# Optimization experiments

Hardware: AMD Instinct MI355X
Metric: run time of the kernel (lower is better)

Reference implementation:

```python
import jax, jax.numpy as jnp
import numpy as np

N, E, H, HEADS, L, B = 16000, 256000, 192, 4, 4, 8
C = H // HEADS
VN, VE, T = 32, 8, 1000


def _sin_emb(t, dim):
    half = dim // 2
    freqs = jnp.exp(-np.log(10000.0) * jnp.arange(half, dtype=jnp.float32) / half)
    ang = t.astype(jnp.float32)[:, None] * freqs[None, :]
    return jnp.concatenate([jnp.sin(ang), jnp.cos(ang)], axis=-1)


def _ln(x, g, b, eps=1e-5):
    mu = jnp.mean(x, -1, keepdims=True)
    var = jnp.mean(jnp.square(x - mu), -1, keepdims=True)
    return (x - mu) * jax.lax.rsqrt(var + eps) * g + b


def setup_inputs():
    key = jax.random.key(0)
    ks = iter(jax.random.split(key, 64))
    p = lambda shape, s=0.02: jax.random.normal(next(ks), shape, jnp.float32) * s
    inp = {}
    inp['node_emb'] = p((VN, H))
    inp['edge_emb'] = p((VE, H))
    inp['time_w1'] = p((H, H)); inp['time_b1'] = jnp.zeros((H,), jnp.float32)
    inp['time_w2'] = p((H, H)); inp['time_b2'] = jnp.zeros((H,), jnp.float32)
    inp['mask_emb'] = p((2, H))
    inp['wq'] = p((L, H, H)); inp['bq'] = jnp.zeros((L, H), jnp.float32)
    inp['wk'] = p((L, H, H)); inp['bk'] = jnp.zeros((L, H), jnp.float32)
    inp['wv'] = p((L, H, H)); inp['bv'] = jnp.zeros((L, H), jnp.float32)
    inp['we'] = p((L, H, H))
    inp['wskip'] = p((L, H, H)); inp['bskip'] = jnp.zeros((L, H), jnp.float32)
    inp['wbeta'] = p((L, 3 * H))
    inp['ln_g'] = jnp.ones((L, H), jnp.float32); inp['ln_b'] = jnp.zeros((L, H), jnp.float32)
    inp['node_out_w'] = p((H, VN)); inp['node_out_b'] = jnp.zeros((VN,), jnp.float32)
    inp['edge_w1'] = p((4 * H, H)); inp['edge_b1'] = jnp.zeros((H,), jnp.float32)
    inp['edge_w2'] = p((H, VE)); inp['edge_b2'] = jnp.zeros((VE,), jnp.float32)
    inp['node_type'] = jax.random.randint(next(ks), (N,), 0, VN)
    inp['edge_type'] = jax.random.randint(next(ks), (E,), 0, VE)
    inp['edge_index'] = jax.random.randint(next(ks), (2, E), 0, N)
    inp['edit_mask'] = jax.random.randint(next(ks), (N,), 0, 2, dtype=jnp.int32)
    inp['node_batch'] = jnp.sort(jax.random.randint(next(ks), (N,), 0, B))
    inp['t_graph'] = jax.random.randint(next(ks), (B,), 1, T)
    return inp


def reference(node_emb, edge_emb, time_w1, time_b1, time_w2, time_b2, mask_emb,
              wq, bq, wk, bk, wv, bv, we, wskip, bskip, wbeta, ln_g, ln_b,
              node_out_w, node_out_b, edge_w1, edge_b1, edge_w2, edge_b2,
              node_type, edge_type, edge_index, edit_mask, node_batch, t_graph):
    src, dst = edge_index[0], edge_index[1]
    # time embedding: sinusoidal -> Linear -> SiLU -> Linear  => [B, H]
    t_vec = jax.nn.silu(_sin_emb(t_graph, H) @ time_w1 + time_b1) @ time_w2 + time_b2
    t_node = t_vec[node_batch]              # [N, H]
    t_edge = t_vec[node_batch[src]]         # [E, H]
    x = node_emb[node_type] + t_node + mask_emb[edit_mask]
    edge_attr = edge_emb[edge_type] + t_edge
    scale = 1.0 / np.sqrt(C)
    for l in range(L):
        q = (x @ wq[l] + bq[l]).reshape(N, HEADS, C)
        k = (x @ wk[l] + bk[l]).reshape(N, HEADS, C)
        v = (x @ wv[l] + bv[l]).reshape(N, HEADS, C)
        e = (edge_attr @ we[l]).reshape(E, HEADS, C)
        kj = k[src] + e                                   # [E, heads, C]
        score = jnp.sum(q[dst] * kj, axis=-1) * scale      # [E, heads]
        m = jax.ops.segment_max(score, dst, num_segments=N)
        ex = jnp.exp(score - m[dst])
        denom = jax.ops.segment_sum(ex, dst, num_segments=N)
        alpha = ex / denom[dst]
        msg = (v[src] + e) * alpha[..., None]              # [E, heads, C]
        out = jax.ops.segment_sum(msg, dst, num_segments=N).reshape(N, H)
        xr = x @ wskip[l] + bskip[l]
        beta = jax.nn.sigmoid(jnp.concatenate([out, xr, out - xr], -1) @ wbeta[l])[:, None]
        h = beta * xr + (1.0 - beta) * out
        x = _ln(x + h, ln_g[l], ln_b[l])
    node_logits = x @ node_out_w + node_out_b
    edge_feat = jnp.concatenate([x[src], x[dst], edge_attr, t_edge], -1)  # [E, 4H]
    edge_logits = jax.nn.silu(edge_feat @ edge_w1 + edge_b1) @ edge_w2 + edge_b2
    return node_logits, edge_logits
```

## Files before the change

kernel.cpp:

```cpp
#include <hip/hip_runtime.h>
#include <hip/hip_bf16.h>
#include <math.h>

#define NN 16000
#define NPAD 16128
#define NE 256000
#define H 192
#define RP 256
#define KVR 512
#define NL 4
#define NBATCH 8
#define VEt 8
#define HH (H*H)
#define EML 16

typedef __hip_bfloat16 bf16;
typedef unsigned short u16;
typedef unsigned char u8;
typedef unsigned int u32;
typedef __attribute__((ext_vector_type(8))) short bfrag_t;
typedef __attribute__((ext_vector_type(4))) float facc_t;
typedef __attribute__((ext_vector_type(4))) float f4;
typedef __attribute__((ext_vector_type(2))) unsigned int u32x2;
typedef __attribute__((ext_vector_type(2))) float f2v;

__device__ __forceinline__ bf16 f2b(float v){ return __float2bfloat16(v); }
__device__ __forceinline__ int rfl(int v){ return __builtin_amdgcn_readfirstlane(v); }

__device__ __forceinline__ unsigned enc8sw(float x){
    unsigned u = __float_as_uint(x);
    unsigned s = (u >> 24) & 0x80u;
    float ax = fabsf(x);
    if(ax >= 448.f) return s | 0x7Eu;
    if(ax < 0.015625f){
        int q = (int)rintf(ax * 512.f);
        return s | (unsigned)q;
    }
    unsigned au = u & 0x7FFFFFFFu;
    unsigned lsb = (au >> 20) & 1u;
    au += 0x7FFFFu + lsb;
    unsigned E = (au >> 23) - 127u;
    unsigned M = (au >> 20) & 7u;
    if((int)E > 8) return s | 0x7Eu;
    return s | ((E + 7u) << 3) | M;
}
__device__ __forceinline__ unsigned enc8(float x){
#if __has_builtin(__builtin_amdgcn_cvt_pk_fp8_f32)
    return (u32)__builtin_amdgcn_cvt_pk_fp8_f32(x, x, 0, false) & 0xFFu;
#else
    return enc8sw(x);
#endif
}
template<int SEL>
__device__ __forceinline__ float dec8s(u32 w){
#if __has_builtin(__builtin_amdgcn_cvt_f32_fp8)
    return __builtin_amdgcn_cvt_f32_fp8((int)w, SEL);
#else
    unsigned v = (w >> (SEL*8)) & 0xFFu;
    unsigned e = (v >> 3) & 15u, m = v & 7u;
    float mag = e ? __builtin_ldexpf((float)(8u + m), (int)e - 10)
                  : __builtin_ldexpf((float)m, -9);
    return (v & 0x80u) ? -mag : mag;
#endif
}
__device__ __forceinline__ f2v dec8pk01(u32 w){
#if __has_builtin(__builtin_amdgcn_cvt_pk_f32_fp8)
    return __builtin_amdgcn_cvt_pk_f32_fp8((int)w, false);
#else
    f2v r; r.x = dec8s<0>(w); r.y = dec8s<1>(w); return r;
#endif
}
__device__ __forceinline__ float frcp(float x){
#if __has_builtin(__builtin_amdgcn_rcpf)
    return __builtin_amdgcn_rcpf(x);
#else
    return 1.f/x;
#endif
}

__global__ void k_sentinel(float* __restrict__ out, float v){ out[0] = v; }

__global__ void k_prep0(const float* __restrict__ wq, const float* __restrict__ wk,
                        const float* __restrict__ wv, const float* __restrict__ wsk,
                        const float* __restrict__ w1, const float* __restrict__ now,
                        const float* __restrict__ ew2, u16* __restrict__ wt,
                        const int* __restrict__ tg, const float* __restrict__ tw1,
                        const float* __restrict__ tb1, const float* __restrict__ tw2,
                        const float* __restrict__ tb2, float* __restrict__ tvec,
                        int* __restrict__ cnt){
    int blk = blockIdx.x;
    if(blk < 160){
        int mat = blk >> 3, ys = blk & 7;
        if(mat < 18){
            const float* src;
            if(mat < 4)       src = wq  + (size_t)mat*HH;
            else if(mat < 8)  src = wk  + (size_t)(mat-4)*HH;
            else if(mat < 12) src = wv  + (size_t)(mat-8)*HH;
            else if(mat < 16) src = wsk + (size_t)(mat-12)*HH;
            else              src = w1  + (size_t)(mat-16)*HH;
            u16* dst = wt + (size_t)mat*HH;
            const int slice = HH/8;
            int base = ys*slice;
            for(int i = base + threadIdx.x; i < base + slice; i += blockDim.x){
                int k = i / H, n = i % H;
                bf16 b = f2b(src[i]);
                dst[n*H + k] = *(u16*)&b;
            }
        } else if(mat == 18){
            u16* dst = wt + (size_t)18*HH;
            const int slice = (32*192)/8;
            int base = ys*slice;
            for(int i = base + threadIdx.x; i < base + slice; i += blockDim.x){
                int k = i >> 5, n = i & 31;
                bf16 b = f2b(now[i]);
                dst[n*192 + k] = *(u16*)&b;
            }
        } else {
            u16* dst = wt + (size_t)18*HH + 32*192;
            const int slice = (16*192)/8;
            int base = ys*slice;
            for(int i = base + threadIdx.x; i < base + slice; i += blockDim.x){
                int k = i >> 4, n = i & 15;
                float v = (n < 8) ? ew2[k*8 + n] : 0.f;
                bf16 b = f2b(v);
                dst[n*192 + k] = *(u16*)&b;
            }
        }
    } else if(blk < 168){
        int b = blk - 160, j = threadIdx.x;
        __shared__ float emb[H], h1[H];
        float t = (float)tg[b];
        if(j < 96){
            float fr = __expf(-logf(10000.0f) * (float)j / 96.0f);
            float ang = t * fr;
            emb[j]      = sinf(ang);
            emb[j + 96] = cosf(ang);
        }
        __syncthreads();
        if(j < H){
            float acc = tb1[j];
            for(int k = 0; k < H; k++) acc += emb[k] * tw1[k*H + j];
            h1[j] = acc / (1.f + __expf(-acc));
        }
        __syncthreads();
        if(j < H){
            float acc2 = tb2[j];
            for(int k = 0; k < H; k++) acc2 += h1[k] * tw2[k*H + j];
            tvec[b*H + j] = acc2;
        }
    } else {
        int i = (blk - 168)*256 + threadIdx.x;
        if(i < NN+1) cnt[i] = 0;
    }
}

__global__ void k_prep1(const float* __restrict__ nemb, const float* __restrict__ memb,
                        const float* __restrict__ tvec, const int* __restrict__ ntype,
                        const int* __restrict__ emask, const int* __restrict__ nbatch,
                        float* __restrict__ x, u16* __restrict__ xb,
                        const int* __restrict__ edst, int* __restrict__ cnt,
                        const float* __restrict__ eemb, const float* __restrict__ we,
                        const float* __restrict__ w1, const float* __restrict__ b1,
                        u16* __restrict__ etab, u16* __restrict__ ctab){
    int blk = blockIdx.x;
    if(blk < 12000){
        int idx = blk*256 + threadIdx.x;
        int n = idx / H, c = idx % H;
        float v = nemb[(size_t)ntype[n]*H + c] + tvec[nbatch[n]*H + c]
                + memb[(size_t)emask[n]*H + c];
        x[idx] = v;
        bf16 b = f2b(v); xb[idx] = *(u16*)&b;
    } else if(blk < 13000){
        int e = (blk - 12000)*256 + threadIdx.x;
        atomicAdd(&cnt[edst[e]], 1);
    } else {
        int blk2 = blk - 13000;
        int c = threadIdx.x;
        __shared__ float a[H];
        if(blk2 < NL*64){
            int l = blk2 >> 6, idx = blk2 & 63, b = idx >> 3, et = idx & 7;
            if(c < H) a[c] = eemb[et*H + c] + tvec[b*H + c];
            __syncthreads();
            if(c < H){
                float acc = 0.f;
                const float* w = we + (size_t)l*HH;
                for(int k = 0; k < H; k++) acc += a[k] * w[k*H + c];
                bf16 bv = f2b(acc);
                etab[(size_t)blk2*256 + (c/3)*4 + (c%3)] = *(u16*)&bv;
            }
        } else {
            int idx = blk2 - NL*64, b = idx >> 3, et = idx & 7;
            if(c < H) a[c] = eemb[et*H + c] + tvec[b*H + c];
            __syncthreads();
            if(c < H){
                float acc = b1[c];
                for(int k = 0; k < H; k++){
                    acc += a[k]          * w1[(size_t)(2*H + k)*H + c];
                    acc += tvec[b*H + k] * w1[(size_t)(3*H + k)*H + c];
                }
                bf16 bv = f2b(acc);
                ctab[(size_t)idx*256 + (c/3)*4 + (c%3)] = *(u16*)&bv;
            }
        }
    }
}

__global__ __launch_bounds__(1024) void k_scan(const int* __restrict__ cnt,
                                               int* __restrict__ ofs, int* __restrict__ cur){
    __shared__ int wsum[16];
    __shared__ int carry_s;
    int tid = threadIdx.x, lane = tid & 63, w = tid >> 6;
    if(tid == 0) carry_s = 0;
    __syncthreads();
    for(int base = 0; base < NN; base += 1024){
        int idx = base + tid;
        int v = (idx < NN) ? cnt[idx] : 0;
        int sc = v;
        #pragma unroll
        for(int o = 1; o < 64; o <<= 1){
            int t = __shfl_up(sc, o);
            if(lane >= o) sc += t;
        }
        if(lane == 63) wsum[w] = sc;
        __syncthreads();
        if(w == 0){
            int ws = (lane < 16) ? wsum[lane] : 0;
            #pragma unroll
            for(int o = 1; o < 16; o <<= 1){
                int t = __shfl_up(ws, o);
                if(lane >= o) ws += t;
            }
            if(lane < 16) wsum[lane] = ws;
        }
        __syncthreads();
        int wbase = (w > 0) ? wsum[w-1] : 0;
        int c = carry_s;
        int excl = c + wbase + sc - v;
        if(idx < NN){ ofs[idx] = excl; cur[idx] = excl; }
        __syncthreads();
        if(tid == 0) carry_s = c + wsum[15];
        __syncthreads();
    }
    if(threadIdx.x == 0) ofs[NN] = carry_s;
}
__global__ void k_scatter(const int* __restrict__ esrc, const int* __restrict__ edst,
                          const int* __restrict__ etype, const int* __restrict__ nbatch,
                          int* __restrict__ cur, int2* __restrict__ spair, int4* __restrict__ eprep){
    int e = blockIdx.x*blockDim.x + threadIdx.x;
    if(e >= NE) return;
    int s = esrc[e], d = edst[e];
    int ct = (nbatch[s]*VEt + etype[e])*KVR;
    int pos = atomicAdd(&cur[d], 1);
    int2 se; se.x = s*KVR; se.y = ct;
    spair[pos] = se;
    eprep[e] = make_int4(s*RP, d*RP, ct, 0);
}

struct GemmP {
    const u16* wt[4];
    const float* bias[4];
    void* out[4];
    int obf[4];
};
__global__ __launch_bounds__(256) void k_gemm(const u16* __restrict__ A, GemmP P){
    int oi = blockIdx.y / 3, nt = blockIdx.y % 3;
    const u16* Wt = P.wt[oi];
    const float* bias = P.bias[oi];
    int wave = rfl(threadIdx.x >> 6), lane = threadIdx.x & 63;
    int quad = lane >> 4, l16 = lane & 15;
    int m0 = blockIdx.x*256 + wave*64;
    int n0 = nt*64;
    facc_t acc[4][4];
    #pragma unroll
    for(int i = 0; i < 4; i++)
        #pragma unroll
        for(int j = 0; j < 4; j++){ acc[i][j][0]=0.f; acc[i][j][1]=0.f; acc[i][j][2]=0.f; acc[i][j][3]=0.f; }
    #pragma unroll
    for(int kc = 0; kc < 6; kc++){
        int kb = kc*32 + quad*8;
        bfrag_t af[4], bg[4];
        #pragma unroll
        for(int i = 0; i < 4; i++) af[i] = *(const bfrag_t*)(A  + (size_t)(m0 + i*16 + l16)*H + kb);
        #pragma unroll
        for(int j = 0; j < 4; j++) bg[j] = *(const bfrag_t*)(Wt + (size_t)(n0 + j*16 + l16)*H + kb);
        #pragma unroll
        for(int i = 0; i < 4; i++)
            #pragma unroll
            for(int j = 0; j < 4; j++)
                acc[i][j] = __builtin_amdgcn_mfma_f32_16x16x32_bf16(af[i], bg[j], acc[i][j], 0, 0, 0);
    }
    float bv[4];
    #pragma unroll
    for(int j = 0; j < 4; j++) bv[j] = bias ? bias[n0 + j*16 + l16] : 0.f;
    int mode = P.obf[oi];
    if(mode == 5){
        u16* outp = (u16*)P.out[oi];
        int hoff[4];
        #pragma unroll
        for(int j = 0; j < 4; j++){
            int c = n0 + j*16 + l16;
            hoff[j] = (c/3)*4 + (c%3);
        }
        #pragma unroll
        for(int i = 0; i < 4; i++){
            int rb = m0 + i*16 + quad*4;
            #pragma unroll
            for(int r = 0; r < 4; r++){
                int row = rb + r;
                if(row < NN){
                    #pragma unroll
                    for(int j = 0; j < 4; j++){
                        bf16 b = f2b(acc[i][j][r] + bv[j]);
                        outp[(size_t)row*256 + hoff[j]] = *(u16*)&b;
                    }
                }
            }
        }
    } else if(mode != 0){
        u8* out = (u8*)P.out[oi];
        int rstride = (mode == 2) ? RP : KVR;
        int mult    = (mode == 2) ? 4  : 8;
        int koff    = (mode == 4) ? 4  : 0;
        int byteoff[4];
        #pragma unroll
        for(int j = 0; j < 4; j++){
            int c = n0 + j*16 + l16;
            byteoff[j] = (c/3)*mult + (c%3) + koff;
        }
        #pragma unroll
        for(int i = 0; i < 4; i++){
            int rb = m0 + i*16 + quad*4;
            #pragma unroll
            for(int r = 0; r < 4; r++){
                int row = rb + r;
                if(row < NN){
                    #pragma unroll
                    for(int j = 0; j < 4; j++)
                        out[(size_t)row*rstride + byteoff[j]] = (u8)enc8(acc[i][j][r] + bv[j]);
                }
            }
        }
    } else {
        float* out = (float*)P.out[oi];
        #pragma unroll
        for(int i = 0; i < 4; i++){
            int rb = m0 + i*16 + quad*4;
            #pragma unroll
            for(int r = 0; r < 4; r++){
                int row = rb + r;
                if(row < NN){
                    #pragma unroll
                    for(int j = 0; j < 4; j++)
                        out[(size_t)row*H + n0 + j*16 + l16] = acc[i][j][r] + bv[j];
                }
            }
        }
    }
}

__global__ __launch_bounds__(256) void k_attn(
    const u8* __restrict__ Qb, const u8* __restrict__ KVb,
    const float* __restrict__ XR,
    const u16* __restrict__ etab, const int* __restrict__ ofs,
    const int2* __restrict__ spair,
    const float* __restrict__ wb, const float* __restrict__ lng, const float* __restrict__ lnb,
    float* __restrict__ x, u16* __restrict__ xb)
{
    int wv = rfl(threadIdx.x >> 6);
    int n = blockIdx.x*4 + wv;
    int lane = threadIdx.x & 63;
    int lane8 = lane*8;
    int ch = lane*3;
    size_t base = (size_t)n*H + ch;
    const float scale = 0.14433756729740646f;
    u32x2 qw = *(const u32x2*)(Qb + (size_t)n*512 + lane8);
    float q0 = __uint_as_float(qw.x << 16);
    float q1 = __uint_as_float(qw.x & 0xffff0000u);
    float q2 = __uint_as_float(qw.y << 16);
    int p0 = ofs[n], p1 = ofs[n+1];
    float lac[4]  = {0.f,0.f,0.f,0.f};
    float ac0[4]  = {0.f,0.f,0.f,0.f};
    float ac1[4]  = {0.f,0.f,0.f,0.f};
    float ac2[4]  = {0.f,0.f,0.f,0.f};
    const u8* etb = (const u8*)etab;
    int p = p0;
    u32x2 kvc[4], ewc[4];
    bool have = (p + 3 < p1);
    if(have){
        #pragma unroll
        for(int t = 0; t < 4; t++){
            int2 se = spair[p+t];
            kvc[t] = *(const u32x2*)(KVb + se.x + lane8);
            ewc[t] = *(const u32x2*)(etb + se.y + lane8);
        }
    }
    while(have){
        int pn = p + 4;
        bool more = (pn + 3 < p1);
        u32x2 kvn[4], ewn[4];
        if(more){
            #pragma unroll
            for(int t = 0; t < 4; t++){
                int2 se = spair[pn+t];
                kvn[t] = *(const u32x2*)(KVb + se.x + lane8);
                ewn[t] = *(const u32x2*)(etb + se.y + lane8);
            }
        }
        float e0[4], e1[4], e2[4], tt[4];
        #pragma unroll
        for(int t = 0; t < 4; t++){
            e0[t] = __uint_as_float(ewc[t].x << 16);
            e1[t] = __uint_as_float(ewc[t].x & 0xffff0000u);
            e2[t] = __uint_as_float(ewc[t].y << 16);
            f2v k01 = dec8pk01(kvc[t].x);
            float k2 = dec8s<2>(kvc[t].x);
            tt[t] = q0*(k01.x+e0[t]) + q1*(k01.y+e1[t]) + q2*(k2+e2[t]);
        }
        #pragma unroll
        for(int o = 1; o <= 8; o <<= 1){
            #pragma unroll
            for(int t = 0; t < 4; t++) tt[t] += __shfl_xor(tt[t], o);
        }
        #pragma unroll
        for(int t = 0; t < 4; t++){
            float sc = fminf(fmaxf(tt[t]*scale, -60.f), 60.f);
            float pw = __expf(sc);
            f2v v01 = dec8pk01(kvc[t].y);
            float v2 = dec8s<2>(kvc[t].y);
            lac[t] += pw;
            ac0[t] += pw*(v01.x+e0[t]);
            ac1[t] += pw*(v01.y+e1[t]);
            ac2[t] += pw*(v2+e2[t]);
        }
        if(more){
            #pragma unroll
            for(int t = 0; t < 4; t++){ kvc[t] = kvn[t]; ewc[t] = ewn[t]; }
        }
        p = pn;
        have = more;
    }
    for(; p < p1; p++){
        int soA = spair[p].x, eoA = spair[p].y;
        u32x2 kvA = *(const u32x2*)(KVb + soA + lane8);
        u32x2 ewA = *(const u32x2*)(etb + eoA + lane8);
        float e0A = __uint_as_float(ewA.x << 16);
        float e1A = __uint_as_float(ewA.x & 0xffff0000u);
        float e2A = __uint_as_float(ewA.y << 16);
        f2v k01 = dec8pk01(kvA.x);
        float k2 = dec8s<2>(kvA.x);
        float tA = q0*(k01.x+e0A) + q1*(k01.y+e1A) + q2*(k2+e2A);
        tA += __shfl_xor(tA,1); tA += __shfl_xor(tA,2); tA += __shfl_xor(tA,4); tA += __shfl_xor(tA,8);
        float sc = fminf(fmaxf(tA*scale, -60.f), 60.f);
        float pw = __expf(sc);
        f2v v01 = dec8pk01(kvA.y);
        float v2 = dec8s<2>(kvA.y);
        lac[0] += pw;
        ac0[0] += pw*(v01.x+e0A);
        ac1[0] += pw*(v01.y+e1A);
        ac2[0] += pw*(v2+e2A);
    }
    float l  = (lac[0]+lac[1]) + (lac[2]+lac[3]);
    float a0 = (ac0[0]+ac0[1]) + (ac0[2]+ac0[3]);
    float a1 = (ac1[0]+ac1[1]) + (ac1[2]+ac1[3]);
    float a2 = (ac2[0]+ac2[1]) + (ac2[2]+ac2[3]);
    float inv = (p1 > p0) ? 1.f/l : 0.f;
    float o0 = a0*inv, o1 = a1*inv, o2 = a2*inv;
    float xr0 = XR[base], xr1 = XR[base+1], xr2 = XR[base+2];
    float sd = o0*wb[ch]  + o1*wb[ch+1]  + o2*wb[ch+2]
             + xr0*wb[H+ch] + xr1*wb[H+ch+1] + xr2*wb[H+ch+2]
             + (o0-xr0)*wb[2*H+ch] + (o1-xr1)*wb[2*H+ch+1] + (o2-xr2)*wb[2*H+ch+2];
    sd += __shfl_xor(sd,1); sd += __shfl_xor(sd,2); sd += __shfl_xor(sd,4);
    sd += __shfl_xor(sd,8); sd += __shfl_xor(sd,16); sd += __shfl_xor(sd,32);
    float beta = 1.f/(1.f + __expf(-sd));
    float h0 = beta*xr0 + (1.f-beta)*o0;
    float h1 = beta*xr1 + (1.f-beta)*o1;
    float h2 = beta*xr2 + (1.f-beta)*o2;
    float y0 = x[base] + h0, y1 = x[base+1] + h1, y2 = x[base+2] + h2;
    float s3 = y0 + y1 + y2;
    float q3 = y0*y0 + y1*y1 + y2*y2;
    #pragma unroll
    for(int o = 1; o <= 32; o <<= 1){
        s3 += __shfl_xor(s3, o);
        q3 += __shfl_xor(q3, o);
    }
    float mean = s3 * (1.f/H);
    float var = fmaxf(q3*(1.f/H) - mean*mean, 0.f);
    float rs = rsqrtf(var + 1e-5f);
    float d0 = y0-mean, d1 = y1-mean, d2 = y2-mean;
    float z0 = d0*rs*lng[ch]   + lnb[ch];
    float z1 = d1*rs*lng[ch+1] + lnb[ch+1];
    float z2 = d2*rs*lng[ch+2] + lnb[ch+2];
    x[base] = z0; x[base+1] = z1; x[base+2] = z2;
    bf16 t0 = f2b(z0), t1 = f2b(z1), t2 = f2b(z2);
    xb[base] = *(u16*)&t0; xb[base+1] = *(u16*)&t1; xb[base+2] = *(u16*)&t2;
}

__global__ __launch_bounds__(256) void k_nodeout(const u16* __restrict__ A, const u16* __restrict__ Wt,
                                                 const float* __restrict__ b, float* __restrict__ out){
    int wave = rfl(threadIdx.x >> 6), lane = threadIdx.x & 63;
    int quad = lane >> 4, l16 = lane & 15;
    int m0 = blockIdx.x*256 + wave*64;
    facc_t acc[4][2];
    #pragma unroll
    for(int i = 0; i < 4; i++)
        #pragma unroll
        for(int j = 0; j < 2; j++){ acc[i][j][0]=0.f; acc[i][j][1]=0.f; acc[i][j][2]=0.f; acc[i][j][3]=0.f; }
    #pragma unroll
    for(int kc = 0; kc < 6; kc++){
        int kb = kc*32 + quad*8;
        bfrag_t af[4], bg[2];
        #pragma unroll
        for(int i = 0; i < 4; i++) af[i] = *(const bfrag_t*)(A  + (size_t)(m0 + i*16 + l16)*H + kb);
        #pragma unroll
        for(int j = 0; j < 2; j++) bg[j] = *(const bfrag_t*)(Wt + (size_t)(j*16 + l16)*H + kb);
        #pragma unroll
        for(int i = 0; i < 4; i++)
            #pragma unroll
            for(int j = 0; j < 2; j++)
                acc[i][j] = __builtin_amdgcn_mfma_f32_16x16x32_bf16(af[i], bg[j], acc[i][j], 0, 0, 0);
    }
    float bv[2];
    #pragma unroll
    for(int j = 0; j < 2; j++) bv[j] = b[j*16 + l16];
    #pragma unroll
    for(int i = 0; i < 4; i++){
        int rb = m0 + i*16 + quad*4;
        #pragma unroll
        for(int r = 0; r < 4; r++){
            int row = rb + r;
            if(row < NN){
                #pragma unroll
                for(int j = 0; j < 2; j++)
                    out[(size_t)row*32 + j*16 + l16] = acc[i][j][r] + bv[j];
            }
        }
    }
}

__global__ __launch_bounds__(256) void k_edgemlp(
    const int4* __restrict__ eprep,
    const u8* __restrict__ xs1, const u8* __restrict__ xd1, const u16* __restrict__ ctab,
    const u16* __restrict__ w2t, const float* __restrict__ b2p, float* __restrict__ out)
{
    __shared__ u16 hbuf[4][16][200];
    int wave = rfl(threadIdx.x >> 6);
    int lane = threadIdx.x & 63;
    int lane8 = lane*8;
    int l16 = lane & 15, quad = lane >> 4;
    int wid = blockIdx.x*4 + wave;
    int e0 = wid*EML;
    const u8* ctb = (const u8*)ctab;
    bfrag_t bg[6];
    #pragma unroll
    for(int kc = 0; kc < 6; kc++)
        bg[kc] = *(const bfrag_t*)(w2t + (size_t)l16*192 + kc*32 + quad*8);
    for(int eb = 0; eb < EML; eb += 2){
        int4 epX = eprep[e0 + eb];
        int4 epY = eprep[e0 + eb + 1];
        u32 awX = *(const u32*)(xs1 + epX.x + lane*4);
        u32 awY = *(const u32*)(xs1 + epY.x + lane*4);
        u32 bwX = *(const u32*)(xd1 + epX.y + lane*4);
        u32 bwY = *(const u32*)(xd1 + epY.y + lane*4);
        u32x2 cwX = *(const u32x2*)(ctb + epX.z + lane8);
        u32x2 cwY = *(const u32x2*)(ctb + epY.z + lane8);
        float cfX0 = __uint_as_float(cwX.x << 16);
        float cfX1 = __uint_as_float(cwX.x & 0xffff0000u);
        float cfX2 = __uint_as_float(cwX.y << 16);
        float cfY0 = __uint_as_float(cwY.x << 16);
        float cfY1 = __uint_as_float(cwY.x & 0xffff0000u);
        float cfY2 = __uint_as_float(cwY.y << 16);
        f2v aX = dec8pk01(awX), bX = dec8pk01(bwX);
        f2v aY = dec8pk01(awY), bY = dec8pk01(bwY);
        float aX2 = dec8s<2>(awX), bX2 = dec8s<2>(bwX);
        float aY2 = dec8s<2>(awY), bY2 = dec8s<2>(bwY);
        float hX0, hX1, hX2, hY0, hY1, hY2;
        { float v = aX.x+bX.x+cfX0; hX0 = v*frcp(1.f+__expf(-v)); }
        { float v = aX.y+bX.y+cfX1; hX1 = v*frcp(1.f+__expf(-v)); }
        { float v = aX2 +bX2 +cfX2; hX2 = v*frcp(1.f+__expf(-v)); }
        { float v = aY.x+bY.x+cfY0; hY0 = v*frcp(1.f+__expf(-v)); }
        { float v = aY.y+bY.y+cfY1; hY1 = v*frcp(1.f+__expf(-v)); }
        { float v = aY2 +bY2 +cfY2; hY2 = v*frcp(1.f+__expf(-v)); }
        u16* rowX = &hbuf[wave][eb][0];
        u16* rowY = &hbuf[wave][eb+1][0];
        bf16 x0 = f2b(hX0), x1 = f2b(hX1), x2 = f2b(hX2);
        bf16 y0 = f2b(hY0), y1 = f2b(hY1), y2 = f2b(hY2);
        rowX[lane*3+0] = *(u16*)&x0; rowX[lane*3+1] = *(u16*)&x1; rowX[lane*3+2] = *(u16*)&x2;
        rowY[lane*3+0] = *(u16*)&y0; rowY[lane*3+1] = *(u16*)&y1; rowY[lane*3+2] = *(u16*)&y2;
    }
    __syncthreads();
    facc_t acc;
    acc[0]=0.f; acc[1]=0.f; acc[2]=0.f; acc[3]=0.f;
    #pragma unroll
    for(int kc = 0; kc < 6; kc++){
        bfrag_t af = *(const bfrag_t*)&hbuf[wave][l16][kc*32 + quad*8];
        acc = __builtin_amdgcn_mfma_f32_16x16x32_bf16(af, bg[kc], acc, 0, 0, 0);
    }
    if(l16 < 8){
        float bo = b2p[l16];
        #pragma unroll
        for(int r = 0; r < 4; r++){
            int e = e0 + quad*4 + r;
            out[(size_t)e*8 + l16] = acc[r] + bo;
        }
    }
}

extern "C" void kernel_launch(void* const* d_in, const int* in_sizes, int n_in,
                              void* d_out, int out_size, void* d_ws, size_t ws_size,
                              hipStream_t stream)
{
    {
        int bad = -1;
        if(n_in != 31) bad = 100;
        else {
            const int chk_idx[9] = {0, 7, 16, 21, 23, 26, 27, 29, 30};
            const int chk_sz [9] = {32*H, NL*HH, NL*3*H, 4*HH, H*8, NE, 2*NE, NN, NBATCH};
            for(int i = 0; i < 9; i++) if(in_sizes[chk_idx[i]] != chk_sz[i]){ bad = chk_idx[i]; break; }
        }
        if(bad >= 0){ k_sentinel<<<1,1,0,stream>>>((float*)d_out, 20000.f + 256.f*bad); return; }
        if(out_size != NN*32 + NE*8){ k_sentinel<<<1,1,0,stream>>>((float*)d_out, 30000.f); return; }
    }

    const float* node_emb = (const float*)d_in[0];
    const float* edge_emb = (const float*)d_in[1];
    const float* time_w1  = (const float*)d_in[2];
    const float* time_b1  = (const float*)d_in[3];
    const float* time_w2  = (const float*)d_in[4];
    const float* time_b2  = (const float*)d_in[5];
    const float* mask_emb = (const float*)d_in[6];
    const float* wq       = (const float*)d_in[7];
    const float* bq       = (const float*)d_in[8];
    const float* wk       = (const float*)d_in[9];
    const float* bk       = (const float*)d_in[10];
    const float* wv       = (const float*)d_in[11];
    const float* bv       = (const float*)d_in[12];
    const float* we       = (const float*)d_in[13];
    const float* wskip    = (const float*)d_in[14];
    const float* bskip    = (const float*)d_in[15];
    const float* wbeta    = (const float*)d_in[16];
    const float* ln_g     = (const float*)d_in[17];
    const float* ln_b     = (const float*)d_in[18];
    const float* now      = (const float*)d_in[19];
    const float* nob      = (const float*)d_in[20];
    const float* ew1      = (const float*)d_in[21];
    const float* eb1      = (const float*)d_in[22];
    const float* ew2      = (const float*)d_in[23];
    const float* eb2      = (const float*)d_in[24];
    const int* node_type  = (const int*)d_in[25];
    const int* edge_type  = (const int*)d_in[26];
    const int* edge_index = (const int*)d_in[27];
    const int* edit_mask  = (const int*)d_in[28];
    const int* node_batch = (const int*)d_in[29];
    const int* t_graph    = (const int*)d_in[30];
    const int* esrc = edge_index;
    const int* edst = edge_index + NE;

    char* wsb = (char*)d_ws;
    size_t off = 0;
    auto take = [&](size_t bytes) -> char* {
        char* r = wsb + off;
        off += (bytes + 255) & ~(size_t)255;
        return r;
    };
    float* tvec = (float*)take((size_t)NBATCH*H*4);
    float* x    = (float*)take((size_t)NN*H*4);
    u16*   xb   = (u16*)  take((size_t)NPAD*H*2);
    u8*    Qb   = (u8*)   take((size_t)NN*512);
    u8*    KVb  = (u8*)   take((size_t)NN*KVR);
    float* XR   = (float*)take((size_t)NN*H*4);
    u8*    xs1  = (u8*)   take((size_t)NN*RP);
    u8*    xd1  = (u8*)   take((size_t)NN*RP);
    u16*   etab = (u16*)  take((size_t)NL*64*KVR);
    u16*   ctab = (u16*)  take((size_t)64*KVR);
    u16*   wt   = (u16*)  take((size_t)(18*HH + 32*192 + 16*192)*2);
    int* cnt    = (int*)  take((size_t)(NN+1)*4);
    int* offa   = (int*)  take((size_t)(NN+1)*4);
    int* cur    = (int*)  take((size_t)(NN+1)*4);
    int2* spair = (int2*) take((size_t)NE*8);
    int4* eprep = (int4*) take((size_t)NE*16);

    if(ws_size < off){
        k_sentinel<<<1,1,0,stream>>>((float*)d_out, 10000.f + (float)(ws_size >> 20));
        return;
    }

    u16* w32t = wt + (size_t)18*HH;
    u16* w2t  = w32t + 32*192;

    k_prep0<<<231, 256, 0, stream>>>(wq, wk, wv, wskip, ew1, now, ew2, wt,
                                     t_graph, time_w1, time_b1, time_w2, time_b2, tvec, cnt);
    k_prep1<<<13320, 256, 0, stream>>>(node_emb, mask_emb, tvec, node_type, edit_mask, node_batch,
                                       x, xb, edst, cnt, edge_emb, we, ew1, eb1, etab, ctab);
    k_scan<<<1, 1024, 0, stream>>>(cnt, offa, cur);
    k_scatter<<<NE/256, 256, 0, stream>>>(esrc, edst, edge_type, node_batch, cur, spair, eprep);

    for(int l = 0; l < NL; l++){
        GemmP P;
        P.wt[0] = wt + (size_t)(0  + l)*HH;  P.bias[0] = bq   + (size_t)l*H;  P.out[0] = Qb;  P.obf[0] = 5;
        P.wt[1] = wt + (size_t)(4  + l)*HH;  P.bias[1] = bk   + (size_t)l*H;  P.out[1] = KVb; P.obf[1] = 3;
        P.wt[2] = wt + (size_t)(8  + l)*HH;  P.bias[2] = bv   + (size_t)l*H;  P.out[2] = KVb; P.obf[2] = 4;
        P.wt[3] = wt + (size_t)(12 + l)*HH;  P.bias[3] = bskip+ (size_t)l*H;  P.out[3] = XR;  P.obf[3] = 0;
        k_gemm<<<dim3(63, 12), 256, 0, stream>>>(xb, P);
        k_attn<<<NN/4, 256, 0, stream>>>(Qb, KVb, XR, etab + (size_t)l*64*256, offa, spair,
                                         wbeta + (size_t)l*3*H, ln_g + (size_t)l*H,
                                         ln_b + (size_t)l*H, x, xb);
    }
    {
        GemmP P;
        P.wt[0] = wt + (size_t)16*HH; P.bias[0] = nullptr; P.out[0] = xs1; P.obf[0] = 2;
        P.wt[1] = wt + (size_t)17*HH; P.bias[1] = nullptr; P.out[1] = xd1; P.obf[1] = 2;
        P.wt[2] = P.wt[0]; P.bias[2] = nullptr; P.out[2] = xs1; P.obf[2] = 2;
        P.wt[3] = P.wt[0]; P.bias[3] = nullptr; P.out[3] = xs1; P.obf[3] = 2;
        k_gemm<<<dim3(63, 6), 256, 0, stream>>>(xb, P);
    }
    k_nodeout<<<63, 256, 0, stream>>>(xb, w32t, nob, (float*)d_out);
    k_edgemlp<<<NE/(4*EML), 256, 0, stream>>>(eprep, xs1, xd1, ctab,
                                              w2t, eb2, (float*)d_out + (size_t)NN*32);
}
```

Before: 459.3 us.

## Store skip projection as packed bf16, vectorize prep, use nontemporal gathers

Result: slower. 508.8 us (+10.8%).

```diff
diff --git a/kernel.cpp b/kernel.cpp
--- a/kernel.cpp
+++ b/kernel.cpp
@@ -76,6 +76,12 @@
 #else
     return 1.f/x;
 #endif
+}
+__device__ __forceinline__ u32x2 ldnt2(const void* p){
+    return __builtin_nontemporal_load((const u32x2*)p);
+}
+__device__ __forceinline__ u32 ldnt1(const void* p){
+    return __builtin_nontemporal_load((const u32*)p);
 }
 
 __global__ void k_sentinel(float* __restrict__ out, float v){ out[0] = v; }
@@ -163,18 +169,23 @@
                         const float* __restrict__ w1, const float* __restrict__ b1,
                         u16* __restrict__ etab, u16* __restrict__ ctab){
     int blk = blockIdx.x;
-    if(blk < 12000){
-        int idx = blk*256 + threadIdx.x;
-        int n = idx / H, c = idx % H;
-        float v = nemb[(size_t)ntype[n]*H + c] + tvec[nbatch[n]*H + c]
-                + memb[(size_t)emask[n]*H + c];
-        x[idx] = v;
-        bf16 b = f2b(v); xb[idx] = *(u16*)&b;
-    } else if(blk < 13000){
-        int e = (blk - 12000)*256 + threadIdx.x;
+    if(blk < 3000){
+        int idx4 = (blk*256 + threadIdx.x)*4;
+        int n = idx4 / H, c = idx4 % H;
+        f4 nv = *(const f4*)(nemb + (size_t)ntype[n]*H + c);
+        f4 tv = *(const f4*)(tvec + (size_t)nbatch[n]*H + c);
+        f4 mv = *(const f4*)(memb + (size_t)emask[n]*H + c);
+        f4 v; v.x = nv.x+tv.x+mv.x; v.y = nv.y+tv.y+mv.y;
+              v.z = nv.z+tv.z+mv.z; v.w = nv.w+tv.w+mv.w;
+        *(f4*)(x + idx4) = v;
+        bf16 b0 = f2b(v.x), b1v = f2b(v.y), b2 = f2b(v.z), b3 = f2b(v.w);
+        u16* xbp = xb + idx4;
+        xbp[0] = *(u16*)&b0; xbp[1] = *(u16*)&b1v; xbp[2] = *(u16*)&b2; xbp[3] = *(u16*)&b3;
+    } else if(blk < 4000){
+        int e = (blk - 3000)*256 + threadIdx.x;
         atomicAdd(&cnt[edst[e]], 1);
     } else {
-        int blk2 = blk - 13000;
+        int blk2 = blk - 4000;
         int c = threadIdx.x;
         __shared__ float a[H];
         if(blk2 < NL*64){
@@ -360,7 +371,7 @@
 
 __global__ __launch_bounds__(256) void k_attn(
     const u8* __restrict__ Qb, const u8* __restrict__ KVb,
-    const float* __restrict__ XR,
+    const u8* __restrict__ XRp,
     const u16* __restrict__ etab, const int* __restrict__ ofs,
     const int2* __restrict__ spair,
     const float* __restrict__ wb, const float* __restrict__ lng, const float* __restrict__ lnb,
@@ -390,7 +401,7 @@
         #pragma unroll
         for(int t = 0; t < 4; t++){
             int2 se = spair[p+t];
-            kvc[t] = *(const u32x2*)(KVb + se.x + lane8);
+            kvc[t] = ldnt2(KVb + se.x + lane8);
             ewc[t] = *(const u32x2*)(etb + se.y + lane8);
         }
     }
@@ -402,7 +413,7 @@
             #pragma unroll
             for(int t = 0; t < 4; t++){
                 int2 se = spair[pn+t];
-                kvn[t] = *(const u32x2*)(KVb + se.x + lane8);
+                kvn[t] = ldnt2(KVb + se.x + lane8);
                 ewn[t] = *(const u32x2*)(etb + se.y + lane8);
             }
         }
@@ -441,7 +452,7 @@
     }
     for(; p < p1; p++){
         int soA = spair[p].x, eoA = spair[p].y;
-        u32x2 kvA = *(const u32x2*)(KVb + soA + lane8);
+        u32x2 kvA = ldnt2(KVb + soA + lane8);
         u32x2 ewA = *(const u32x2*)(etb + eoA + lane8);
         float e0A = __uint_as_float(ewA.x << 16);
         float e1A = __uint_as_float(ewA.x & 0xffff0000u);
@@ -465,7 +476,10 @@
     float a2 = (ac2[0]+ac2[1]) + (ac2[2]+ac2[3]);
     float inv = (p1 > p0) ? 1.f/l : 0.f;
     float o0 = a0*inv, o1 = a1*inv, o2 = a2*inv;
-    float xr0 = XR[base], xr1 = XR[base+1], xr2 = XR[base+2];
+    u32x2 xrw = *(const u32x2*)(XRp + (size_t)n*512 + lane8);
+    float xr0 = __uint_as_float(xrw.x << 16);
+    float xr1 = __uint_as_float(xrw.x & 0xffff0000u);
+    float xr2 = __uint_as_float(xrw.y << 16);
     float sd = o0*wb[ch]  + o1*wb[ch+1]  + o2*wb[ch+2]
              + xr0*wb[H+ch] + xr1*wb[H+ch+1] + xr2*wb[H+ch+2]
              + (o0-xr0)*wb[2*H+ch] + (o1-xr1)*wb[2*H+ch+1] + (o2-xr2)*wb[2*H+ch+2];
@@ -557,10 +571,10 @@
     for(int eb = 0; eb < EML; eb += 2){
         int4 epX = eprep[e0 + eb];
         int4 epY = eprep[e0 + eb + 1];
-        u32 awX = *(const u32*)(xs1 + epX.x + lane*4);
-        u32 awY = *(const u32*)(xs1 + epY.x + lane*4);
-        u32 bwX = *(const u32*)(xd1 + epX.y + lane*4);
-        u32 bwY = *(const u32*)(xd1 + epY.y + lane*4);
+        u32 awX = ldnt1(xs1 + epX.x + lane*4);
+        u32 awY = ldnt1(xs1 + epY.x + lane*4);
+        u32 bwX = ldnt1(xd1 + epX.y + lane*4);
+        u32 bwY = ldnt1(xd1 + epY.y + lane*4);
         u32x2 cwX = *(const u32x2*)(ctb + epX.z + lane8);
         u32x2 cwY = *(const u32x2*)(ctb + epY.z + lane8);
         float cfX0 = __uint_as_float(cwX.x << 16);
@@ -667,7 +681,7 @@
     u16*   xb   = (u16*)  take((size_t)NPAD*H*2);
     u8*    Qb   = (u8*)   take((size_t)NN*512);
     u8*    KVb  = (u8*)   take((size_t)NN*KVR);
-    float* XR   = (float*)take((size_t)NN*H*4);
+    u8*    XRp  = (u8*)   take((size_t)NN*512);
     u8*    xs1  = (u8*)   take((size_t)NN*RP);
     u8*    xd1  = (u8*)   take((size_t)NN*RP);
     u16*   etab = (u16*)  take((size_t)NL*64*KVR);
@@ -689,8 +703,8 @@
 
     k_prep0<<<231, 256, 0, stream>>>(wq, wk, wv, wskip, ew1, now, ew2, wt,
                                      t_graph, time_w1, time_b1, time_w2, time_b2, tvec, cnt);
-    k_prep1<<<13320, 256, 0, stream>>>(node_emb, mask_emb, tvec, node_type, edit_mask, node_batch,
-                                       x, xb, edst, cnt, edge_emb, we, ew1, eb1, etab, ctab);
+    k_prep1<<<4320, 256, 0, stream>>>(node_emb, mask_emb, tvec, node_type, edit_mask, node_batch,
+                                      x, xb, edst, cnt, edge_emb, we, ew1, eb1, etab, ctab);
     k_scan<<<1, 1024, 0, stream>>>(cnt, offa, cur);
     k_scatter<<<NE/256, 256, 0, stream>>>(esrc, edst, edge_type, node_batch, cur, spair, eprep);
 
@@ -699,9 +713,9 @@
         P.wt[0] = wt + (size_t)(0  + l)*HH;  P.bias[0] = bq   + (size_t)l*H;  P.out[0] = Qb;  P.obf[0] = 5;
         P.wt[1] = wt + (size_t)(4  + l)*HH;  P.bias[1] = bk   + (size_t)l*H;  P.out[1] = KVb; P.obf[1] = 3;
         P.wt[2] = wt + (size_t)(8  + l)*HH;  P.bias[2] = bv   + (size_t)l*H;  P.out[2] = KVb; P.obf[2] = 4;
-        P.wt[3] = wt + (size_t)(12 + l)*HH;  P.bias[3] = bskip+ (size_t)l*H;  P.out[3] = XR;  P.obf[3] = 0;
+        P.wt[3] = wt + (size_t)(12 + l)*HH;  P.bias[3] = bskip+ (size_t)l*H;  P.out[3] = XRp; P.obf[3] = 5;
         k_gemm<<<dim3(63, 12), 256, 0, stream>>>(xb, P);
-        k_attn<<<NN/4, 256, 0, stream>>>(Qb, KVb, XR, etab + (size_t)l*64*256, offa, spair,
+        k_attn<<<NN/4, 256, 0, stream>>>(Qb, KVb, XRp, etab + (size_t)l*64*256, offa, spair,
                                          wbeta + (size_t)l*3*H, ln_g + (size_t)l*H,
                                          ln_b + (size_t)l*H, x, xb);
     }
```
